# Kernel tuning notes

Measured on AMD Instinct MI355X. Metric: run time of the kernel, lower is better.

## Reference

```python
import jax, jax.numpy as jnp
import numpy as np

BOX = 256           # box_size
OS = 2              # grid_oversampling_factor
GRID = BOX * OS     # oversampled image size
NPTS = 30000        # n_points
NCLS = 2            # n_classes
NLAT = 16           # n_latent_dims
NLAY = 6            # n_layers
H = 256             # n_neurons_per_layer
L = 10              # pos_enc_dim
BATCH = 4


def positional_encoding(pos, n_freq):
    # NeRF-style: sin/cos(2^k * pi * x) per coordinate -> [N, 6*n_freq]
    freqs = 2.0 ** jnp.arange(n_freq, dtype=pos.dtype)
    ang = pos[..., None] * freqs * jnp.pi                    # [N,3,L]
    enc = jnp.concatenate([jnp.sin(ang), jnp.cos(ang)], axis=-1)
    return enc.reshape(pos.shape[0], 6 * n_freq)


def euler_zyz_to_matrix(ang):
    # ang: [B,3] -> R = Rz(a) @ Ry(b) @ Rz(c), [B,3,3]
    a, b, c = ang[:, 0], ang[:, 1], ang[:, 2]
    ca, sa = jnp.cos(a), jnp.sin(a)
    cb, sb = jnp.cos(b), jnp.sin(b)
    cc, sc = jnp.cos(c), jnp.sin(c)
    row0 = jnp.stack([ca * cb * cc - sa * sc, -ca * cb * sc - sa * cc, ca * sb], -1)
    row1 = jnp.stack([sa * cb * cc + ca * sc, -sa * cb * sc + ca * cc, sa * sb], -1)
    row2 = jnp.stack([-sb * cc, sb * sc, cb], -1)
    return jnp.stack([row0, row1, row2], axis=-2)


def points_to_images(proj, amps):
    # proj: [B,N,2] in [-0.5,0.5]; amps: [B,C,N] -> [B,C,GRID,GRID] via bilinear splat
    B, N, _ = proj.shape
    C = amps.shape[1]
    p = jnp.clip((proj + 0.5) * (GRID - 1), 0.0, GRID - 1.000001)
    x, y = p[..., 0], p[..., 1]
    x0f = jnp.floor(x); y0f = jnp.floor(y)
    fx = x - x0f; fy = y - y0f
    x0 = x0f.astype(jnp.int32); y0 = y0f.astype(jnp.int32)
    x1 = jnp.minimum(x0 + 1, GRID - 1); y1 = jnp.minimum(y0 + 1, GRID - 1)
    w = jnp.stack([(1 - fx) * (1 - fy), fx * (1 - fy), (1 - fx) * fy, fx * fy], -1)  # [B,N,4]
    xi = jnp.stack([x0, x1, x0, x1], -1)
    yi = jnp.stack([y0, y0, y1, y1], -1)
    pix = yi * GRID + xi                                            # [B,N,4]
    bc = (jnp.arange(B)[:, None] * C + jnp.arange(C)[None, :])      # [B,C]
    idx = bc[:, :, None, None] * (GRID * GRID) + pix[:, None, :, :]  # [B,C,N,4]
    vals = amps[:, :, :, None] * w[:, None, :, :]                    # [B,C,N,4]
    img = jnp.zeros((B * C * GRID * GRID,), vals.dtype)
    img = img.at[idx.reshape(-1)].add(vals.reshape(-1))
    return img.reshape(B, C, GRID, GRID)


def fourier_smooth(images, A, B_width):
    # per-class Gaussian low-pass in Fourier, sum classes, crop oversampled grid to BOX
    f = jnp.fft.fftfreq(GRID).astype(images.dtype)
    R = f[None, :] ** 2 + f[:, None] ** 2                            # [G,G]
    filt = A[:, None, None] * jnp.exp(-(B_width[:, None, None] ** 2) * R)
    F = jnp.fft.fft2(images)                                         # [B,C,G,G]
    Fs = jnp.sum(filt * F, axis=1)                                   # [B,G,G]
    Fs = jnp.fft.fftshift(Fs, axes=(-2, -1))
    s = (GRID - BOX) // 2
    Fc = Fs[:, s:s + BOX, s:s + BOX]
    Fc = jnp.fft.ifftshift(Fc, axes=(-2, -1))
    return jnp.real(jnp.fft.ifft2(Fc)) / (OS * OS)


def fourier_shift_2d(im, sx, sy):
    f = jnp.fft.fftfreq(BOX)
    phase = jnp.exp(-2j * jnp.pi * (sx[:, None, None] * f[None, None, :]
                                    + sy[:, None, None] * f[None, :, None]))
    return jnp.real(jnp.fft.ifft2(jnp.fft.fft2(im) * phase))


def setup_inputs() -> dict:
    key = jax.random.key(0)
    ks = jax.random.split(key, 10)
    din = 6 * L + NLAT
    return {
        "z": jax.random.normal(ks[0], (BATCH, NLAT), jnp.float32),
        "orientation": jax.random.uniform(ks[1], (BATCH, 3), jnp.float32, 0.0, 2.0 * np.pi),
        "shift": jax.random.normal(ks[2], (BATCH, 2), jnp.float32) * 2.0,
        "model_positions": jax.random.uniform(ks[3], (NPTS, 3), jnp.float32, -0.4, 0.4),
        "amp": 50.0 * jnp.ones((NCLS, NPTS), jnp.float32),
        "ampvar": jax.random.normal(ks[4], (NCLS, NPTS), jnp.float32),
        "W_in": jax.random.normal(ks[5], (din, H), jnp.float32) / np.sqrt(din),
        "W_layers": jax.random.normal(ks[6], (NLAY, H, H), jnp.float32) / np.sqrt(H),
        "W_out1": jax.random.normal(ks[7], (H, 3), jnp.float32) / np.sqrt(H),
        "W_out2": jax.random.normal(ks[8], (3, 3), jnp.float32) * 0.01,
        "A": jnp.ones((NCLS,), jnp.float32),
        "B_width": 5.0 * jnp.ones((NCLS,), jnp.float32),
    }


def reference(z, orientation, shift, model_positions, amp, ampvar,
              W_in, W_layers, W_out1, W_out2, A, B_width):
    B = z.shape[0]
    # --- displacement MLP (mask=None, warmup=False path) ---
    enc = positional_encoding(model_positions, L)                    # [N,6L]
    feat = jnp.concatenate([
        jnp.broadcast_to(enc[None], (B, NPTS, 6 * L)),
        jnp.broadcast_to(z[:, None, :], (B, NPTS, NLAT)),
    ], axis=-1)                                                      # [B,N,6L+lat]
    h = feat @ W_in                                                  # input Linear (no bias)
    for i in range(NLAY):                                            # LinearBlock = ELU(Linear)
        h = jax.nn.elu(h @ W_layers[i])
    disp = jax.nn.elu(h @ W_out1) @ W_out2                           # [B,N,3]
    final_pos = model_positions[None] + disp                         # [B,N,3]
    # --- projection ---
    Rm = euler_zyz_to_matrix(orientation)                            # [B,3,3]
    proj = jnp.einsum('bnd,bde->bne', final_pos, Rm)[..., :2]        # [B,N,2]
    # --- amplitudes, splat, smooth, shift ---
    wamp = amp * jax.nn.softmax(ampvar, axis=0)                      # [C,N]
    wamp = jnp.broadcast_to(wamp[None], (B, NCLS, NPTS))
    imgs = points_to_images(proj, wamp)                              # [B,C,G,G]
    sm = fourier_smooth(imgs, A, B_width)                            # [B,BOX,BOX]
    out = fourier_shift_2d(sm, shift[:, 0], shift[:, 1])
    return out, final_pos, disp
```

## Files before the change

### kernel.cpp

```cpp
#include <hip/hip_runtime.h>

#define PI_F 3.14159265358979323846f

constexpr int GRIDN = 512;
constexpr int BOXN  = 256;
constexpr int NPTS  = 30000;
constexpr int NCLS  = 2;
constexpr int NLAT  = 16;
constexpr int HDIM  = 256;
constexpr int LFREQ = 10;
constexpr int BATCH = 4;
constexpr int NROWS = BATCH*NPTS;
constexpr int RM    = 48;

#define ASC   2048.0f
#define AINV  (1.0f/2048.0f)
#define OINV  (1.0f/33554432.0f)
#define BSC   16384.0f

typedef _Float16 f16x8 __attribute__((ext_vector_type(8)));
typedef float    f32x4 __attribute__((ext_vector_type(4)));

__device__ __forceinline__ float elu_f(float x){ return x > 0.f ? x : (__expf(x) - 1.0f); }

__device__ __forceinline__ void split_f16(float vs, uint32_t& hb, uint32_t& lb){
    const _Float16 h = (_Float16)vs;
    const _Float16 l = (_Float16)(vs - (float)h);
    union { _Float16 f; uint16_t u; } uh, ul;
    uh.f = h; ul.f = l;
    hb = uh.u; lb = ul.u;
}
__device__ __forceinline__ uint32_t pack_act(float v){
    uint32_t hb, lb;
    split_f16(v * ASC, hb, lb);
    return hb | (lb << 16);
}
__device__ __forceinline__ float unpack_act(uint32_t u){
    union { uint16_t u16; _Float16 f; } a, b;
    a.u16 = (uint16_t)(u & 0xffffu);
    b.u16 = (uint16_t)(u >> 16);
    return ((float)a.f + (float)b.f) * AINV;
}

__host__ __device__ __forceinline__ size_t wp_off(int lay){
    return (lay == 0) ? 0 : (size_t)(98304 + (lay-1)*262144);
}

__global__ void prepack_kernel(const float* __restrict__ Win,
                               const float* __restrict__ Wlay,
                               unsigned char* __restrict__ wp)
{
    const int tid = blockIdx.x*256 + threadIdx.x;
    if (tid >= 7*8*16*64) return;
    const int lane  = tid & 63;
    const int n16   = (tid >> 6) & 15;
    const int kstep = (tid >> 10) & 7;
    const int lay   = tid >> 13;
    if (lay == 0 && kstep >= 3) return;
    const int kbase = 32*kstep + 8*(lane >> 4);
    const int c = 16*n16 + (lane & 15);
    uint32_t hw[4], lw[4];
    #pragma unroll
    for (int p = 0; p < 4; ++p) {
        uint32_t hh0=0, hh1=0, ll0=0, ll1=0;
        #pragma unroll
        for (int q = 0; q < 2; ++q) {
            const int k = kbase + 2*p + q;
            float w = 0.f;
            if (lay == 0) { if (k < 76) w = Win[k*HDIM + c]; }
            else w = Wlay[(size_t)(lay-1)*HDIM*HDIM + (size_t)k*HDIM + c];
            uint32_t hb, lb;
            split_f16(w * BSC, hb, lb);
            if (q == 0) { hh0 = hb; ll0 = lb; } else { hh1 = hb; ll1 = lb; }
        }
        hw[p] = hh0 | (hh1 << 16);
        lw[p] = ll0 | (ll1 << 16);
    }
    uint4* dst = (uint4*)(wp + wp_off(lay)) + (size_t)((kstep*16 + n16)*2)*64 + lane;
    dst[0]  = make_uint4(hw[0], hw[1], hw[2], hw[3]);
    dst[64] = make_uint4(lw[0], lw[1], lw[2], lw[3]);
}

__launch_bounds__(512, 4)
__global__ void mlp_fused(const float* __restrict__ pos,
                          const float* __restrict__ zlat,
                          const unsigned char* __restrict__ wp,
                          const float* __restrict__ Wout1,
                          const float* __restrict__ Wout2,
                          const float* __restrict__ orient,
                          const float* __restrict__ amp,
                          const float* __restrict__ ampvar,
                          float* __restrict__ out_fp,
                          float* __restrict__ out_disp,
                          float* __restrict__ img)
{
    __shared__ uint4 h4[RM*64];
    __shared__ float w1s[HDIM*3];
    uint32_t* hs = (uint32_t*)h4;
    const int t = threadIdx.x;
    const int lane = t & 63;
    const int wv = t >> 6;
    const int row0 = blockIdx.x * RM;
    const int g  = lane >> 4;
    const int rb = lane & 15;

    for (int idx = t; idx < RM*96; idx += 512) {
        const int r = idx / 96, c = idx - r*96;
        const int row = row0 + r;
        const int b = row / NPTS, n = row - b*NPTS;
        float v = 0.f;
        if (c < 60) {
            const int d = c / 20, rem = c - d*20;
            const int f = (rem < 10) ? rem : rem - 10;
            const float ang = pos[n*3+d] * (float)(1<<f) * PI_F;
            v = (rem < 10) ? sinf(ang) : cosf(ang);
        } else if (c < 76) {
            v = zlat[b*NLAT + (c - 60)];
        }
        hs[r*256 + (c ^ ((r&7)<<2))] = pack_act(v);
    }
    for (int idx = t; idx < HDIM*3; idx += 512) w1s[idx] = Wout1[idx];
    __syncthreads();

    for (int lay = 0; lay < 7; ++lay) {
        const int KS = lay ? 8 : 3;
        const uint4* bp = (const uint4*)(wp + wp_off(lay));

        f32x4 acc[6];
        #pragma unroll
        for (int i = 0; i < 6; ++i) { f32x4 zz = {0.f,0.f,0.f,0.f}; acc[i] = zz; }

        uint4 BH0[2], BL0[2], BH1[2], BL1[2];

        auto LOADB = [&](uint4 (&H)[2], uint4 (&L)[2], int k){
            #pragma unroll
            for (int f = 0; f < 2; ++f) {
                const size_t s0 = (size_t)((k*16 + 2*wv + f)*2)*64 + lane;
                H[f] = bp[s0];
                L[f] = bp[s0 + 64];
            }
        };
        auto STEP = [&](const uint4 (&H)[2], const uint4 (&L)[2], int k){
            #pragma unroll
            for (int m = 0; m < 3; ++m) {
                const int r = 16*m + rb;
                const int s = r & 7;
                const int G0 = 8*k + 2*g;
                const uint4 p0 = h4[r*64 + (G0 ^ s)];
                const uint4 p1 = h4[r*64 + ((G0+1) ^ s)];
                const uint32_t e0=p0.x, e1=p0.y, e2=p0.z, e3=p0.w;
                const uint32_t e4=p1.x, e5=p1.y, e6=p1.z, e7=p1.w;
                union { uint4 q; f16x8 v; } ah, al;
                ah.q = make_uint4((e0 & 0xffffu) | (e1 << 16),
                                  (e2 & 0xffffu) | (e3 << 16),
                                  (e4 & 0xffffu) | (e5 << 16),
                                  (e6 & 0xffffu) | (e7 << 16));
                al.q = make_uint4((e0 >> 16) | (e1 & 0xffff0000u),
                                  (e2 >> 16) | (e3 & 0xffff0000u),
                                  (e4 >> 16) | (e5 & 0xffff0000u),
                                  (e6 >> 16) | (e7 & 0xffff0000u));
                #pragma unroll
                for (int nn = 0; nn < 2; ++nn) {
                    union { uint4 q; f16x8 v; } bh, bl;
                    bh.q = H[nn]; bl.q = L[nn];
                    f32x4 a = acc[m*2+nn];
                    a = __builtin_amdgcn_mfma_f32_16x16x32_f16(ah.v, bl.v, a, 0, 0, 0);
                    a = __builtin_amdgcn_mfma_f32_16x16x32_f16(al.v, bh.v, a, 0, 0, 0);
                    a = __builtin_amdgcn_mfma_f32_16x16x32_f16(ah.v, bh.v, a, 0, 0, 0);
                    acc[m*2+nn] = a;
                }
            }
        };

        LOADB(BH0, BL0, 0);
        for (int k = 0; k < KS; k += 2) {
            if (k+1 < KS) LOADB(BH1, BL1, k+1);
            STEP(BH0, BL0, k);
            if (k+1 < KS) {
                if (k+2 < KS) LOADB(BH0, BL0, k+2);
                STEP(BH1, BL1, k+1);
            }
        }

        __syncthreads();
        const bool do_elu = (lay >= 1);
        #pragma unroll
        for (int m = 0; m < 3; ++m) {
            #pragma unroll
            for (int nn = 0; nn < 2; ++nn) {
                #pragma unroll
                for (int j = 0; j < 4; ++j) {
                    float v = acc[m*2+nn][j] * OINV;
                    if (do_elu) v = elu_f(v);
                    const int r = 16*m + 4*g + j;
                    const int c = 32*wv + 16*nn + rb;
                    hs[r*256 + (c ^ ((r&7)<<2))] = pack_act(v);
                }
            }
        }
        __syncthreads();
    }

    {
        const int r = t >> 2;
        const int q = t & 3;
        if (r < RM) {
            const int s = (r & 7) << 2;
            const uint32_t* hr = hs + r*256;
            float o0=0.f, o1=0.f, o2=0.f;
            #pragma unroll 8
            for (int kk = 0; kk < 64; ++kk) {
                const int k = 64*q + kk;
                const float hv = unpack_act(hr[k ^ s]);
                o0 = fmaf(hv, w1s[k*3+0], o0);
                o1 = fmaf(hv, w1s[k*3+1], o1);
                o2 = fmaf(hv, w1s[k*3+2], o2);
            }
            o0 += __shfl_xor(o0, 1); o0 += __shfl_xor(o0, 2);
            o1 += __shfl_xor(o1, 1); o1 += __shfl_xor(o1, 2);
            o2 += __shfl_xor(o2, 1); o2 += __shfl_xor(o2, 2);
            if (q == 0) {
                const int row = row0 + r;
                const int b = row / NPTS, n = row - b*NPTS;
                o0 = elu_f(o0); o1 = elu_f(o1); o2 = elu_f(o2);
                const float d0 = o0*Wout2[0] + o1*Wout2[3] + o2*Wout2[6];
                const float d1 = o0*Wout2[1] + o1*Wout2[4] + o2*Wout2[7];
                const float d2 = o0*Wout2[2] + o1*Wout2[5] + o2*Wout2[8];
                const float p0 = pos[n*3+0] + d0;
                const float p1 = pos[n*3+1] + d1;
                const float p2 = pos[n*3+2] + d2;
                out_disp[(size_t)row*3+0] = d0; out_disp[(size_t)row*3+1] = d1; out_disp[(size_t)row*3+2] = d2;
                out_fp[(size_t)row*3+0]   = p0; out_fp[(size_t)row*3+1]   = p1; out_fp[(size_t)row*3+2]   = p2;
                float sa,ca,sb,cb,sc,cc;
                sincosf(orient[b*3+0], &sa, &ca);
                sincosf(orient[b*3+1], &sb, &cb);
                sincosf(orient[b*3+2], &sc, &cc);
                const float R00 =  ca*cb*cc - sa*sc;
                const float R10 =  sa*cb*cc + ca*sc;
                const float R20 = -sb*cc;
                const float R01 = -ca*cb*sc - sa*cc;
                const float R11 = -sa*cb*sc + ca*cc;
                const float R21 =  sb*sc;
                const float prx = p0*R00 + p1*R10 + p2*R20;
                const float pry = p0*R01 + p1*R11 + p2*R21;

                float x = (prx + 0.5f) * (float)(GRIDN-1);
                float y = (pry + 0.5f) * (float)(GRIDN-1);
                x = fminf(fmaxf(x, 0.f), 511.0f);
                y = fminf(fmaxf(y, 0.f), 511.0f);
                const float x0f = floorf(x), y0f = floorf(y);
                const float fx = x - x0f, fy = y - y0f;
                const int x0 = (int)x0f, y0 = (int)y0f;
                const int x1 = min(x0+1, GRIDN-1), y1 = min(y0+1, GRIDN-1);
                const float av0 = ampvar[n], av1 = ampvar[NPTS + n];
                const float mx = fmaxf(av0, av1);
                const float e0 = __expf(av0 - mx), e1 = __expf(av1 - mx);
                const float inv = 1.0f / (e0 + e1);
                const float w0 = amp[n]        * e0 * inv;
                const float w1 = amp[NPTS + n] * e1 * inv;
                const float w00 = (1.f-fx)*(1.f-fy), w10 = fx*(1.f-fy), w01 = (1.f-fx)*fy, w11 = fx*fy;
                float* img0 = img + (size_t)(b*NCLS + 0)*GRIDN*GRIDN;
                float* img1 = img + (size_t)(b*NCLS + 1)*GRIDN*GRIDN;
                const int i00 = y0*GRIDN + x0, i10 = y0*GRIDN + x1;
                const int i01 = y1*GRIDN + x0, i11 = y1*GRIDN + x1;
                atomicAdd(img0 + i00, w0*w00); atomicAdd(img0 + i10, w0*w10);
                atomicAdd(img0 + i01, w0*w01); atomicAdd(img0 + i11, w0*w11);
                atomicAdd(img1 + i00, w1*w00); atomicAdd(img1 + i10, w1*w10);
                atomicAdd(img1 + i01, w1*w01); atomicAdd(img1 + i11, w1*w11);
            }
        }
    }
}

__global__ void fft_row_pair(const float* __restrict__ img, float2* __restrict__ Z)
{
    __shared__ float2 s[512];
    const int t  = threadIdx.x;
    const int rb = blockIdx.x;
    const int b  = rb >> 9, y = rb & 511;
    const float* p0 = img + ((size_t)(b*2+0) << 18) + (size_t)y*512;
    const float* p1 = img + ((size_t)(b*2+1) << 18) + (size_t)y*512;
    #pragma unroll
    for (int j = 0; j < 2; ++j) {
        const int i  = t + j*256;
        const int ri = (int)(__brev((unsigned)i) >> 23);
        s[ri] = make_float2(p0[i], p1[i]);
    }
    for (int len = 1; len < 512; len <<= 1) {
        __syncthreads();
        const int p  = t & (len-1);
        const int i0 = ((t & ~(len-1)) << 1) | p;
        const float ang = -PI_F * (float)p / (float)len;
        float sn, cs; __sincosf(ang, &sn, &cs);
        const float2 a  = s[i0];
        const float2 bv = s[i0 + len];
        const float2 bt = make_float2(bv.x*cs - bv.y*sn, bv.x*sn + bv.y*cs);
        s[i0]       = make_float2(a.x + bt.x, a.y + bt.y);
        s[i0 + len] = make_float2(a.x - bt.x, a.y - bt.y);
    }
    __syncthreads();
    float2* zo = Z + ((size_t)b << 18) + (size_t)y*512;
    #pragma unroll
    for (int j = 0; j < 2; ++j) {
        const int i = t + j*256;
        zo[i] = s[i];
    }
}

template<int N, bool INV, bool RIN, bool ROUT>
__global__ void fft_pass(const float* __restrict__ in, float* __restrict__ out,
                         int in_per, long in_s1, long in_s2, long in_es,
                         int out_per, long out_s1, long out_s2, long out_es,
                         float scale)
{
    __shared__ float2 s[N];
    const int t  = threadIdx.x;
    const int rb = blockIdx.x;
    const long ib = (long)(rb / in_per) * in_s1 + (long)(rb % in_per) * in_s2;
    constexpr int LOG2N = (N == 512) ? 9 : 8;
    #pragma unroll
    for (int j = 0; j < 2; ++j) {
        const int i  = t + j*(N/2);
        const int ri = (int)(__brev((unsigned)i) >> (32 - LOG2N));
        float2 v;
        if (RIN) { v.x = in[ib + (long)i*in_es]; v.y = 0.f; }
        else       v = ((const float2*)in)[ib + (long)i*in_es];
        s[ri] = v;
    }
    for (int len = 1; len < N; len <<= 1) {
        __syncthreads();
        const int p  = t & (len-1);
        const int i0 = ((t & ~(len-1)) << 1) | p;
        const float ang = (INV ? PI_F : -PI_F) * (float)p / (float)len;
        float sn, cs; __sincosf(ang, &sn, &cs);
        const float2 a  = s[i0];
        const float2 bv = s[i0 + len];
        const float2 bt = make_float2(bv.x*cs - bv.y*sn, bv.x*sn + bv.y*cs);
        s[i0]       = make_float2(a.x + bt.x, a.y + bt.y);
        s[i0 + len] = make_float2(a.x - bt.x, a.y - bt.y);
    }
    __syncthreads();
    const long ob = (long)(rb / out_per) * out_s1 + (long)(rb % out_per) * out_s2;
    #pragma unroll
    for (int j = 0; j < 2; ++j) {
        const int i = t + j*(N/2);
        if (ROUT) out[ob + (long)i*out_es] = s[i].x * scale;
        else {
            float2 v = s[i]; v.x *= scale; v.y *= scale;
            ((float2*)out)[ob + (long)i*out_es] = v;
        }
    }
}

__global__ void combine_kernel(const float2* __restrict__ Z,
                               const float* __restrict__ Afac,
                               const float* __restrict__ Bw,
                               const float* __restrict__ shift,
                               float2* __restrict__ Q)
{
    const int u = blockIdx.x;
    const int b = blockIdx.y;
    const int v = threadIdx.x;
    const int mu  = (u < 128) ? u : u + 256;
    const int mv  = (v < 128) ? v : v + 256;
    const int u2  = (256 - u) & 255;
    const int v2  = (256 - v) & 255;
    const int mu2 = (u2 < 128) ? u2 : u2 + 256;
    const int mv2 = (v2 < 128) ? v2 : v2 + 256;
    const int nmu  = (512 - mu)  & 511;
    const int nmv  = (512 - mv)  & 511;
    const int nmu2 = (512 - mu2) & 511;
    const int nmv2 = (512 - mv2) & 511;

    const float2* Zb = Z + ((size_t)b << 18);
    const float2 A   = Zb[(size_t)mu  *512 + mv ];
    const float2 Am  = Zb[(size_t)nmu *512 + nmv];
    const float2 A2  = Zb[(size_t)mu2 *512 + mv2];
    const float2 A2m = Zb[(size_t)nmu2*512 + nmv2];

    float2 F1v[2], FHv[2];
    F1v[0] = make_float2(0.5f*(A.x + Am.x),  0.5f*(A.y - Am.y));
    F1v[1] = make_float2(0.5f*(A.y + Am.y), -0.5f*(A.x - Am.x));
    FHv[0] = make_float2(0.5f*(A2.x + A2m.x),  0.5f*(A2.y - A2m.y));
    FHv[1] = make_float2(0.5f*(A2.y + A2m.y), -0.5f*(A2.x - A2m.x));

    const float fy1 = (float)((mu  < 256) ? mu  : mu  - 512) / 512.0f;
    const float fx1 = (float)((mv  < 256) ? mv  : mv  - 512) / 512.0f;
    const float fy2 = (float)((mu2 < 256) ? mu2 : mu2 - 512) / 512.0f;
    const float fx2 = (float)((mv2 < 256) ? mv2 : mv2 - 512) / 512.0f;
    const float R1 = fy1*fy1 + fx1*fx1;
    const float R2 = fy2*fy2 + fx2*fx2;
    float a1x=0.f, a1y=0.f, a2x=0.f, a2y=0.f;
    #pragma unroll
    for (int c = 0; c < NCLS; ++c) {
        const float bw = Bw[c];
        const float f1 = Afac[c] * __expf(-bw*bw*R1);
        const float f2 = Afac[c] * __expf(-bw*bw*R2);
        a1x = fmaf(f1, F1v[c].x, a1x); a1y = fmaf(f1, F1v[c].y, a1y);
        a2x = fmaf(f2, FHv[c].x, a2x); a2y = fmaf(f2, FHv[c].y, a2y);
    }
    const float Gx = 0.5f*(a1x + a2x);
    const float Gy = 0.5f*(a1y - a2y);
    const float fu = (float)((u < 128) ? u : u - 256) / 256.0f;
    const float fv = (float)((v < 128) ? v : v - 256) / 256.0f;
    const float th = -2.0f*PI_F*(shift[b*2+0]*fv + shift[b*2+1]*fu);
    float sn, cs; __sincosf(th, &sn, &cs);
    float2 o;
    o.x = Gx*cs - Gy*sn;
    o.y = Gx*sn + Gy*cs;
    Q[((size_t)b << 16) + (size_t)u*256 + v] = o;
}

extern "C" void kernel_launch(void* const* d_in, const int* in_sizes, int n_in,
                              void* d_out, int out_size, void* d_ws, size_t ws_size,
                              hipStream_t stream)
{
    (void)in_sizes; (void)n_in; (void)out_size; (void)ws_size;
    const float* z      = (const float*)d_in[0];
    const float* orient = (const float*)d_in[1];
    const float* shift  = (const float*)d_in[2];
    const float* pos    = (const float*)d_in[3];
    const float* amp    = (const float*)d_in[4];
    const float* ampvar = (const float*)d_in[5];
    const float* Win    = (const float*)d_in[6];
    const float* Wlay   = (const float*)d_in[7];
    const float* Wout1  = (const float*)d_in[8];
    const float* Wout2  = (const float*)d_in[9];
    const float* Afac   = (const float*)d_in[10];
    const float* Bw     = (const float*)d_in[11];

    float* out      = (float*)d_out;
    float* out_img  = out;
    float* out_fp   = out + (size_t)BATCH*BOXN*BOXN;
    float* out_disp = out_fp + (size_t)NROWS*3;

    char*   ws   = (char*)d_ws;
    float*  img  = (float*)ws;
    float2* Zb   = (float2*)(ws + (size_t)8*1024*1024);
    unsigned char* wp = (unsigned char*)(ws + (size_t)8*1024*1024);
    float2* Q    = (float2*)(ws + (size_t)25165824);

    (void)hipMemsetAsync(img, 0, (size_t)BATCH*NCLS*GRIDN*GRIDN*sizeof(float), stream);

    prepack_kernel<<<(7*8*16*64 + 255)/256, 256, 0, stream>>>(Win, Wlay, wp);

    mlp_fused<<<NROWS/RM, 512, 0, stream>>>(pos, z, wp, Wout1, Wout2, orient,
                                            amp, ampvar, out_fp, out_disp, img);

    fft_row_pair<<<BATCH*512, 256, 0, stream>>>(img, Zb);
    fft_pass<512,false,false,false><<<BATCH*512, 256, 0, stream>>>(
        (const float*)Zb, (float*)Zb, 512, 262144, 1, 512, 512, 262144, 1, 512, 1.0f);

    combine_kernel<<<dim3(256, BATCH), 256, 0, stream>>>(Zb, Afac, Bw, shift, Q);

    fft_pass<256,true ,false,false><<<BATCH*256, 128, 0, stream>>>(
        (const float*)Q, (float*)Q, 256, 65536, 256, 1, 256, 65536, 256, 1, 1.0f/256.0f);
    fft_pass<256,true ,false,true ><<<BATCH*256, 128, 0, stream>>>(
        (const float*)Q, out_img, 256, 65536, 1, 256, 256, 65536, 1, 256, 0.25f/256.0f);
}
```

Before: 427.0 us.

## Use packed hi/lo activation pairs directly as MFMA operands, dropping split shuffles

After: 501.1 us. 1.17x slower.

```diff
diff --git a/kernel.cpp b/kernel.cpp
--- a/kernel.cpp
+++ b/kernel.cpp
@@ -43,7 +43,7 @@
 }
 
 __host__ __device__ __forceinline__ size_t wp_off(int lay){
-    return (lay == 0) ? 0 : (size_t)(98304 + (lay-1)*262144);
+    return (lay == 0) ? 0 : (size_t)(6*16*2048 + (size_t)(lay-1)*16*16*2048);
 }
 
 __global__ void prepack_kernel(const float* __restrict__ Win,
@@ -51,34 +51,30 @@
                                unsigned char* __restrict__ wp)
 {
     const int tid = blockIdx.x*256 + threadIdx.x;
-    if (tid >= 7*8*16*64) return;
-    const int lane  = tid & 63;
-    const int n16   = (tid >> 6) & 15;
-    const int kstep = (tid >> 10) & 7;
-    const int lay   = tid >> 13;
-    if (lay == 0 && kstep >= 3) return;
-    const int kbase = 32*kstep + 8*(lane >> 4);
+    if (tid >= 102*16*64) return;
+    const int lane = tid & 63;
+    const int n16  = (tid >> 6) & 15;
+    const int widx = tid >> 10;
+    int lay, wi;
+    if (widx < 6) { lay = 0; wi = widx; }
+    else          { lay = 1 + (widx-6)/16; wi = (widx-6) & 15; }
+    const int g = lane >> 4;
     const int c = 16*n16 + (lane & 15);
-    uint32_t hw[4], lw[4];
+    uint32_t b1[4], b3[4];
     #pragma unroll
     for (int p = 0; p < 4; ++p) {
-        uint32_t hh0=0, hh1=0, ll0=0, ll1=0;
-        #pragma unroll
-        for (int q = 0; q < 2; ++q) {
-            const int k = kbase + 2*p + q;
-            float w = 0.f;
-            if (lay == 0) { if (k < 76) w = Win[k*HDIM + c]; }
-            else w = Wlay[(size_t)(lay-1)*HDIM*HDIM + (size_t)k*HDIM + c];
-            uint32_t hb, lb;
-            split_f16(w * BSC, hb, lb);
-            if (q == 0) { hh0 = hb; ll0 = lb; } else { hh1 = hb; ll1 = lb; }
-        }
-        hw[p] = hh0 | (hh1 << 16);
-        lw[p] = ll0 | (ll1 << 16);
-    }
-    uint4* dst = (uint4*)(wp + wp_off(lay)) + (size_t)((kstep*16 + n16)*2)*64 + lane;
-    dst[0]  = make_uint4(hw[0], hw[1], hw[2], hw[3]);
-    dst[64] = make_uint4(lw[0], lw[1], lw[2], lw[3]);
+        const int kap = 16*wi + 4*g + p;
+        float w = 0.f;
+        if (lay == 0) { if (kap < 76) w = Win[kap*HDIM + c]; }
+        else w = Wlay[(size_t)(lay-1)*HDIM*HDIM + (size_t)kap*HDIM + c];
+        uint32_t hb, lb;
+        split_f16(w * BSC, hb, lb);
+        b1[p] = hb | (hb << 16);
+        b3[p] = lb | (lb << 16);
+    }
+    uint4* dst = (uint4*)(wp + wp_off(lay)) + (size_t)(wi*16 + n16)*128 + lane;
+    dst[0]  = make_uint4(b1[0], b1[1], b1[2], b1[3]);
+    dst[64] = make_uint4(b3[0], b3[1], b3[2], b3[3]);
 }
 
 __launch_bounds__(512, 4)
@@ -123,62 +119,50 @@
     __syncthreads();
 
     for (int lay = 0; lay < 7; ++lay) {
-        const int KS = lay ? 8 : 3;
+        const int NW = lay ? 16 : 6;
         const uint4* bp = (const uint4*)(wp + wp_off(lay));
 
         f32x4 acc[6];
         #pragma unroll
         for (int i = 0; i < 6; ++i) { f32x4 zz = {0.f,0.f,0.f,0.f}; acc[i] = zz; }
 
-        uint4 BH0[2], BL0[2], BH1[2], BL1[2];
-
-        auto LOADB = [&](uint4 (&H)[2], uint4 (&L)[2], int k){
-            #pragma unroll
-            for (int f = 0; f < 2; ++f) {
-                const size_t s0 = (size_t)((k*16 + 2*wv + f)*2)*64 + lane;
-                H[f] = bp[s0];
-                L[f] = bp[s0 + 64];
-            }
+        uint4 a10, a11, a30, a31;
+        uint4 b10, b11, b30, b31;
+
+        auto LOADW = [&](uint4& q10, uint4& q11, uint4& q30, uint4& q31, int wi){
+            const size_t s0 = (size_t)(wi*16 + 2*wv)*128 + lane;
+            q10 = bp[s0];
+            q30 = bp[s0 + 64];
+            q11 = bp[s0 + 128];
+            q31 = bp[s0 + 192];
         };
-        auto STEP = [&](const uint4 (&H)[2], const uint4 (&L)[2], int k){
+        auto STEP = [&](const uint4& q10, const uint4& q11, const uint4& q30, const uint4& q31, int wi){
+            union { uint4 q; f16x8 v; } c10, c11, c30, c31;
+            c10.q = q10; c11.q = q11; c30.q = q30; c31.q = q31;
             #pragma unroll
             for (int m = 0; m < 3; ++m) {
                 const int r = 16*m + rb;
                 const int s = r & 7;
-                const int G0 = 8*k + 2*g;
-                const uint4 p0 = h4[r*64 + (G0 ^ s)];
-                const uint4 p1 = h4[r*64 + ((G0+1) ^ s)];
-                const uint32_t e0=p0.x, e1=p0.y, e2=p0.z, e3=p0.w;
-                const uint32_t e4=p1.x, e5=p1.y, e6=p1.z, e7=p1.w;
-                union { uint4 q; f16x8 v; } ah, al;
-                ah.q = make_uint4((e0 & 0xffffu) | (e1 << 16),
-                                  (e2 & 0xffffu) | (e3 << 16),
-                                  (e4 & 0xffffu) | (e5 << 16),
-                                  (e6 & 0xffffu) | (e7 << 16));
-                al.q = make_uint4((e0 >> 16) | (e1 & 0xffff0000u),
-                                  (e2 >> 16) | (e3 & 0xffff0000u),
-                                  (e4 >> 16) | (e5 & 0xffff0000u),
-                                  (e6 >> 16) | (e7 & 0xffff0000u));
-                #pragma unroll
-                for (int nn = 0; nn < 2; ++nn) {
-                    union { uint4 q; f16x8 v; } bh, bl;
-                    bh.q = H[nn]; bl.q = L[nn];
-                    f32x4 a = acc[m*2+nn];
-                    a = __builtin_amdgcn_mfma_f32_16x16x32_f16(ah.v, bl.v, a, 0, 0, 0);
-                    a = __builtin_amdgcn_mfma_f32_16x16x32_f16(al.v, bh.v, a, 0, 0, 0);
-                    a = __builtin_amdgcn_mfma_f32_16x16x32_f16(ah.v, bh.v, a, 0, 0, 0);
-                    acc[m*2+nn] = a;
-                }
+                union { uint4 q; f16x8 v; } A;
+                A.q = h4[r*64 + ((4*wi + g) ^ s)];
+                f32x4 a0 = acc[m*2+0];
+                a0 = __builtin_amdgcn_mfma_f32_16x16x32_f16(A.v, c10.v, a0, 0, 0, 0);
+                a0 = __builtin_amdgcn_mfma_f32_16x16x32_f16(A.v, c30.v, a0, 0, 0, 0);
+                acc[m*2+0] = a0;
+                f32x4 a1 = acc[m*2+1];
+                a1 = __builtin_amdgcn_mfma_f32_16x16x32_f16(A.v, c11.v, a1, 0, 0, 0);
+                a1 = __builtin_amdgcn_mfma_f32_16x16x32_f16(A.v, c31.v, a1, 0, 0, 0);
+                acc[m*2+1] = a1;
             }
         };
 
-        LOADB(BH0, BL0, 0);
-        for (int k = 0; k < KS; k += 2) {
-            if (k+1 < KS) LOADB(BH1, BL1, k+1);
-            STEP(BH0, BL0, k);
-            if (k+1 < KS) {
-                if (k+2 < KS) LOADB(BH0, BL0, k+2);
-                STEP(BH1, BL1, k+1);
+        LOADW(a10, a11, a30, a31, 0);
+        for (int wi = 0; wi < NW; wi += 2) {
+            if (wi+1 < NW) LOADW(b10, b11, b30, b31, wi+1);
+            STEP(a10, a11, a30, a31, wi);
+            if (wi+1 < NW) {
+                if (wi+2 < NW) LOADW(a10, a11, a30, a31, wi+2);
+                STEP(b10, b11, b30, b31, wi+1);
             }
         }
 
@@ -442,7 +426,7 @@
 
     (void)hipMemsetAsync(img, 0, (size_t)BATCH*NCLS*GRIDN*GRIDN*sizeof(float), stream);
 
-    prepack_kernel<<<(7*8*16*64 + 255)/256, 256, 0, stream>>>(Win, Wlay, wp);
+    prepack_kernel<<<(102*16*64 + 255)/256, 256, 0, stream>>>(Win, Wlay, wp);
 
     mlp_fused<<<NROWS/RM, 512, 0, stream>>>(pos, z, wp, Wout1, Wout2, orient,
                                             amp, ampvar, out_fp, out_disp, img);
```
